# Performance work log

Measured on AMD Instinct MI355X. Metric: run time of the kernel, lower is better.

The kernel has to match this reference:

```python
import jax, jax.numpy as jnp
import numpy as np

B, P, D, H, L = 16384, 16, 49, 8, 6
NUM_CLASSES = 10
EPS = 1e-5


def _layernorm(x, w, b):
    mu = jnp.mean(x, axis=-1, keepdims=True)
    var = jnp.mean(jnp.square(x - mu), axis=-1, keepdims=True)
    return (x - mu) * jax.lax.rsqrt(var + EPS) * w + b


def setup_inputs() -> dict:
    key = jax.random.key(0)
    ks = iter(jax.random.split(key, 64))
    s = 0.05
    inp = {
        "x": jax.random.normal(next(ks), (B, P, D), jnp.float32),
        "trg": jax.random.randint(next(ks), (B,), 0, NUM_CLASSES, jnp.int32),
        "patch_proj_w": jax.random.normal(next(ks), (D, D)) * s,
        "patch_proj_b": jnp.zeros((D,)),
        "pos_enc": jax.random.normal(next(ks), (1, P, D)) * 0.02,
        # per-head per-layer attention weights, each head uses full dim D (as in source)
        "Wq": jax.random.normal(next(ks), (L, H, D, D)) * s,
        "bq": jnp.zeros((L, H, D)),
        "Wk": jax.random.normal(next(ks), (L, H, D, D)) * s,
        "bk": jnp.zeros((L, H, D)),
        "Wv": jax.random.normal(next(ks), (L, H, D, D)) * s,
        "bv": jnp.zeros((L, H, D)),
        "Wh": jax.random.normal(next(ks), (L, H, D, D)) * s,
        "bh": jnp.zeros((L, H, D)),
        "Wo": jax.random.normal(next(ks), (L, H * D, D)) * s,
        "bo": jnp.zeros((L, D)),
        "ln1_w": jnp.ones((L, D)), "ln1_b": jnp.zeros((L, D)),
        "ln2_w": jnp.ones((L, D)), "ln2_b": jnp.zeros((L, D)),
        "ffn1_w": jax.random.normal(next(ks), (L, D, 4 * D)) * s,
        "ffn1_b": jnp.zeros((L, 4 * D)),
        "ffn2_w": jax.random.normal(next(ks), (L, 4 * D, D)) * s,
        "ffn2_b": jnp.zeros((L, D)),
        "mlp_w1": jax.random.normal(next(ks), (D, D)) * s, "mlp_b1": jnp.zeros((D,)),
        "mlp_w2": jax.random.normal(next(ks), (D, D)) * s, "mlp_b2": jnp.zeros((D,)),
        "cls_w1": jax.random.normal(next(ks), (D, 25)) * s, "cls_b1": jnp.zeros((25,)),
        "cls_w2": jax.random.normal(next(ks), (25, NUM_CLASSES)) * s, "cls_b2": jnp.zeros((NUM_CLASSES,)),
    }
    return inp


def reference(x, trg, patch_proj_w, patch_proj_b, pos_enc,
              Wq, bq, Wk, bk, Wv, bv, Wh, bh, Wo, bo,
              ln1_w, ln1_b, ln2_w, ln2_b,
              ffn1_w, ffn1_b, ffn2_w, ffn2_b,
              mlp_w1, mlp_b1, mlp_w2, mlp_b2,
              cls_w1, cls_b1, cls_w2, cls_b2):
    b, p, d = x.shape
    h = x @ patch_proj_w + patch_proj_b + pos_enc[:, :p, :]
    scale = 1.0 / jnp.sqrt(jnp.float32(d))  # d_k = dim_proj = 49 per head
    for l in range(Wq.shape[0]):
        # all 8 heads batched: [b,p,d] x [h,d,e] -> [b,h,p,e]
        Q = jnp.einsum('bpd,hde->bhpe', h, Wq[l]) + bq[l][None, :, None, :]
        K = jnp.einsum('bpd,hde->bhpe', h, Wk[l]) + bk[l][None, :, None, :]
        V = jnp.einsum('bpd,hde->bhpe', h, Wv[l]) + bv[l][None, :, None, :]
        attn = jax.nn.softmax(jnp.einsum('bhpe,bhqe->bhpq', Q, K) * scale, axis=-1)
        ao = jnp.einsum('bhpq,bhqe->bhpe', attn, V)
        ho = jnp.einsum('bhpe,heo->bhpo', ao, Wh[l]) + bh[l][None, :, None, :]
        concat = ho.transpose(0, 2, 1, 3).reshape(b, p, -1)  # head-order concat
        attn_out = concat @ Wo[l] + bo[l]
        y = _layernorm(h + attn_out, ln1_w[l], ln1_b[l])
        ffn = jax.nn.gelu(y @ ffn1_w[l] + ffn1_b[l], approximate=False) @ ffn2_w[l] + ffn2_b[l]
        h = _layernorm(y + ffn, ln2_w[l], ln2_b[l])
        # mlp_between_blocks (shared weights) applied after every block
        h = (h @ mlp_w1 + mlp_b1) @ mlp_w2 + mlp_b2
    pooled = h.mean(axis=1)
    logits = (pooled @ cls_w1 + cls_b1) @ cls_w2 + cls_b2
    logp = jax.nn.log_softmax(logits, axis=-1)
    loss = -jnp.mean(jnp.take_along_axis(logp, trg[:, None].astype(jnp.int32), axis=-1))
    acc = jnp.mean((jnp.argmax(logits, axis=-1) == trg).astype(jnp.float32))
    return loss, acc
```

## Files before the change

### kernel.cpp

```cpp
#include <hip/hip_runtime.h>
#include <hip/hip_bf16.h>

#define DEV __device__ __forceinline__

typedef __attribute__((ext_vector_type(8))) __bf16 bfrag;
typedef __attribute__((ext_vector_type(4))) float  f32x4;

DEV f32x4 mfma32(bfrag a, bfrag b, f32x4 c) {
    return __builtin_amdgcn_mfma_f32_16x16x32_bf16(a, b, c, 0, 0, 0);
}

DEV unsigned short to_bf16(float f) {
    union { __bf16 b; unsigned short u; } cv;
    cv.b = (__bf16)f;
    return cv.u;
}

DEV float bf2f(unsigned short u) {
    union { unsigned int i; float f; } cv;
    cv.i = (unsigned int)u << 16;
    return cv.f;
}

#if defined(__has_builtin)
#if __has_builtin(__builtin_amdgcn_cvt_pk_bf16_f32)
#define HAS_PK_BF16 1
#endif
#endif

DEV unsigned int pk2(float a, float b) {
#ifdef HAS_PK_BF16
    auto r = __builtin_amdgcn_cvt_pk_bf16_f32(a, b);
    unsigned int u;
    __builtin_memcpy(&u, &r, 4);
    return u;
#else
    return (unsigned)to_bf16(a) | ((unsigned)to_bf16(b) << 16);
#endif
}

DEV void store4(unsigned short* p, float v0, float v1, float v2, float v3) {
    typedef __attribute__((ext_vector_type(2))) unsigned int uint2v;
    uint2v q;
    q[0] = pk2(v0, v1);
    q[1] = pk2(v2, v3);
    *reinterpret_cast<uint2v*>(p) = q;
}

DEV float fastrcp(float x) { float r; asm("v_rcp_f32 %0, %1" : "=v"(r) : "v"(x)); return r; }

DEV float gelu(float x) {
    float u = x * fmaf(0.07135481f, x * x, 1.5957691f);
    float e = __expf(-u);
    return x * fastrcp(1.0f + e);
}

namespace cfg {
constexpr size_t OFF_ACC  = 0;
constexpr size_t OFF_WQ   = 512;
constexpr size_t SZ_HEAD  = (size_t)48 * 64 * 64 * 2;
constexpr size_t OFF_WK   = OFF_WQ + SZ_HEAD;
constexpr size_t OFF_WV   = OFF_WK + SZ_HEAD;
constexpr size_t OFF_WHOO = OFF_WV + SZ_HEAD;
constexpr size_t OFF_F1   = OFF_WHOO + SZ_HEAD;
constexpr size_t OFF_F2   = OFF_F1 + (size_t)6 * 208 * 64 * 2;
constexpr size_t OFF_MF   = OFF_F2 + (size_t)6 * 64 * 224 * 2;
constexpr size_t OFF_PP   = OFF_MF + 8192;
constexpr size_t OFF_POSB = OFF_PP + 8192;
}


__global__ void pack_qk(const float* __restrict__ wq, const float* __restrict__ bq,
                        const float* __restrict__ wk, const float* __restrict__ bk,
                        char* __restrict__ ws)
{
    int id = blockIdx.x * 256 + threadIdx.x;
    int lh = id >> 12, pos = id & 4095;
    int n = pos >> 6, k = pos & 63;
    float s = 0.f;
// ... 89 lines not shown
            else if (k == 49) v = f1b[l * 196 + n];
        }
        ((unsigned short*)(ws + cfg::OFF_F1))[id] = to_bf16(v);
        return;
    }
    id -= 6 * 208 * 64;
    if (id < 6 * 64 * 224) {
        int l = id / (64 * 224), rem = id % (64 * 224), n = rem / 224, k = rem % 224;
        float v = 0.f;
        if (n < 49) {
            if (k < 196)       v = f2w[((size_t)l * 196 + k) * 49 + n];
            else if (k == 196) v = f2b[l * 49 + n];
        }
        ((unsigned short*)(ws + cfg::OFF_F2))[id] = to_bf16(v);
        return;
    }
    id -= 6 * 64 * 224;
    if (id < 4096) {
        int n = id >> 6, k = id & 63;
        ((unsigned short*)(ws + cfg::OFF_PP))[id] = to_bf16((n < 49 && k < 49) ? ppw[k * 49 + n] : 0.f);
        return;
    }
    id -= 4096;
    if (id < 1024) {
        int p = id >> 6, e = id & 63;
        ((float*)(ws + cfg::OFF_POSB))[id] = (e < 49) ? pos[p * 49 + e] + ppb[e] : 0.f;
        return;
    }
    id -= 1024;
    if (id < 128) ((float*)(ws + cfg::OFF_ACC))[id] = 0.f;
}


__global__ __launch_bounds__(64, 2)
void vit_main(const float* __restrict__ x, const int* __restrict__ trg,
              const float* __restrict__ cw1, const float* __restrict__ cb1,
              const float* __restrict__ cw2, const float* __restrict__ cb2,
              char* __restrict__ ws)
{
    constexpr int S64 = 72;
    constexpr int SV  = 40;
    constexpr int SP  = 40;
    constexpr int SM  = 232;
    constexpr int TA = 0, TB = 1152, TV = 2304, TP = 4384, MIDO = 1152, EL = 5024;
    __shared__ unsigned short sm[2 * EL];

    const int lane = threadIdx.x;
    const int g = lane >> 4, c = lane & 15;
    const long e0 = (long)blockIdx.x * 2;
    const f32x4 FZ = {0.f, 0.f, 0.f, 0.f};

    const unsigned short* WQK = (const unsigned short*)(ws + cfg::OFF_WQ);
    const unsigned short* WVO = (const unsigned short*)(ws + cfg::OFF_WK);
    const unsigned short* F1 = (const unsigned short*)(ws + cfg::OFF_F1);
    const unsigned short* F2 = (const unsigned short*)(ws + cfg::OFF_F2);
    const unsigned short* MF = (const unsigned short*)(ws + cfg::OFF_MF);
    const unsigned short* PP = (const unsigned short*)(ws + cfg::OFF_PP);
    const float* POSB = (const float*)(ws + cfg::OFF_POSB);
    float* ACC = (float*)(ws + cfg::OFF_ACC);

    #pragma unroll
    for (int u = 0; u < 2; ++u) {
        const float* xb = x + (e0 + u) * 784;
        #pragma unroll
        for (int it = 0; it < 8; ++it) {
            int i = it * 64 + lane;
            int p = i >> 5, ee = (i & 31) * 2;
            float v0 = (ee < 49) ? xb[p * 49 + ee] : 0.f;
            float v1 = (ee + 1 < 49) ? xb[p * 49 + ee + 1] : 0.f;
            *reinterpret_cast<unsigned int*>(&sm[u * EL + TA + p * S64 + ee]) = pk2(v0, v1);
        }
    }
    if (lane < 24) {
        int u2 = lane / 12, r = lane % 12, row = 12 + r / 3, seg = r % 3;
        *(f32x4*)&sm[u2 * EL + TP + row * SP + 16 + seg * 8] = FZ;
    }

    bfrag a_h[2][2];
    auto loadB = [&](int off, bfrag (&af)[2][2]) {
        #pragma unroll
        for (int u = 0; u < 2; ++u)
            #pragma unroll
            for (int kk = 0; kk < 2; ++kk)
                af[u][kk] = *(const bfrag*)&sm[u * EL + off + c * S64 + kk * 32 + g * 8];
    };
    loadB(TA, a_h);

    f32x4 hreg[2][4];
    #pragma unroll
    for (int mt = 0; mt < 4; ++mt) {
        f32x4 t0 = FZ, t1 = FZ;
        #pragma unroll
        for (int kk = 0; kk < 2; ++kk) {
            bfrag w = *(const bfrag*)&PP[(mt * 16 + c) * 64 + kk * 32 + g * 8];
            t0 = mfma32(w, a_h[0][kk], t0);
            t1 = mfma32(w, a_h[1][kk], t1);
        }
        f32x4 pb = *(const f32x4*)&POSB[c * 64 + mt * 16 + 4 * g];
        hreg[0][mt] = t0 + pb;
        hreg[1][mt] = t1 + pb;
    }

    for (int l = 0; l < 6; ++l) {
        #pragma unroll
        for (int u = 0; u < 2; ++u)
            #pragma unroll
            for (int mt = 0; mt < 4; ++mt)
                store4(&sm[u * EL + TA + c * S64 + mt * 16 + 4 * g],
                       hreg[u][mt][0], hreg[u][mt][1], hreg[u][mt][2], hreg[u][mt][3]);
        if (lane < 32) sm[(lane >> 4) * EL + TA + (lane & 15) * S64 + 49] = 0x3F80;
        loadB(TA, a_h);

        #pragma unroll
        for (int u = 0; u < 2; ++u) {
            *(f32x4*)&sm[u * EL + TV + lane * SV + 16] = FZ;
            *(f32x4*)&sm[u * EL + TV + lane * SV + 24] = FZ;
        }

        f32x4 oacc[2][4];
        #pragma unroll
        for (int u = 0; u < 2; ++u)
            #pragma unroll
            for (int mt = 0; mt < 4; ++mt) oacc[u][mt] = FZ;

        for (int hh = 0; hh < 8; ++hh) {
            const int lh = l * 8 + hh;
            const unsigned short* wqk = WQK + (size_t)lh * 4096;
            const unsigned short* wvo = WVO + (size_t)lh * 4096;

            #pragma unroll
            for (int mt = 0; mt < 4; ++mt) {
                f32x4 t0 = FZ, t1 = FZ;
                #pragma unroll
                for (int kk = 0; kk < 2; ++kk) {
                    bfrag wf = *(const bfrag*)&wqk[(mt * 16 + c) * 64 + kk * 32 + g * 8];
                    t0 = mfma32(wf, a_h[0][kk], t0);
                    t1 = mfma32(wf, a_h[1][kk], t1);
                }
                store4(&sm[0 * EL + TB + c * S64 + mt * 16 + 4 * g], t0[0], t0[1], t0[2], t0[3]);
                store4(&sm[1 * EL + TB + c * S64 + mt * 16 + 4 * g], t1[0], t1[1], t1[2], t1[3]);
            }
            #pragma unroll
            for (int nt = 0; nt < 4; ++nt) {
                f32x4 v0 = FZ, v1 = FZ;
                #pragma unroll
                for (int kk = 0; kk < 2; ++kk) {
                    bfrag wvf = *(const bfrag*)&wvo[(nt * 16 + c) * 64 + kk * 32 + g * 8];
                    v0 = mfma32(a_h[0][kk], wvf, v0);
                    v1 = mfma32(a_h[1][kk], wvf, v1);
                }
                store4(&sm[0 * EL + TV + (nt * 16 + c) * SV + 4 * g], v0[0], v0[1], v0[2], v0[3]);
                store4(&sm[1 * EL + TV + (nt * 16 + c) * SV + 4 * g], v1[0], v1[1], v1[2], v1[3]);
            }

            #pragma unroll
            for (int u = 0; u < 2; ++u) {
                f32x4 sc = FZ;
                #pragma unroll
                for (int kk = 0; kk < 2; ++kk) {
                    bfrag akf = *(const bfrag*)&sm[u * EL + TB + c * S64 + kk * 32 + g * 8];
                    sc = mfma32(akf, a_h[u][kk], sc);
                }
                float s0 = sc[0], s1 = sc[1], s2 = sc[2], s3 = sc[3];
                float m = fmaxf(fmaxf(s0, s1), fmaxf(s2, s3));
                m = fmaxf(m, __shfl_xor(m, 16));
                m = fmaxf(m, __shfl_xor(m, 32));
                float p0 = __expf(s0 - m), p1 = __expf(s1 - m);
                float p2 = __expf(s2 - m), p3 = __expf(s3 - m);
                float t = p0 + p1 + p2 + p3;
                t += __shfl_xor(t, 16);
                t += __shfl_xor(t, 32);
                float inv = fastrcp(t);
                store4(&sm[u * EL + TP + c * SP + 4 * g], p0 * inv, p1 * inv, p2 * inv, p3 * inv);
            }

            #pragma unroll
            for (int u = 0; u < 2; ++u) {
                bfrag bp = *(const bfrag*)&sm[u * EL + TP + c * SP + g * 8];
                #pragma unroll
                for (int mt = 0; mt < 4; ++mt) {
                    bfrag uf = *(const bfrag*)&sm[u * EL + TV + (mt * 16 + c) * SV + g * 8];
                    oacc[u][mt] = mfma32(uf, bp, oacc[u][mt]);
                }
            }
        }

        f32x4 yreg[2][4];
        {
            const float* ln1wp = (const float*)(ws + cfg::OFF_POSB + 4096);
            const float* ln1bp = ln1wp + 384;
            #pragma unroll
            for (int u = 0; u < 2; ++u) {
                float z[4][4];
                float s = 0.f, q2 = 0.f;
                #pragma unroll
                for (int mt = 0; mt < 4; ++mt)
                    #pragma unroll
                    for (int r = 0; r < 4; ++r) {
                        float zz = hreg[u][mt][r] + oacc[u][mt][r];
                        z[mt][r] = zz;
                        s += zz;
                        q2 += zz * zz;
                    }
                s += __shfl_xor(s, 16); s += __shfl_xor(s, 32);
                q2 += __shfl_xor(q2, 16); q2 += __shfl_xor(q2, 32);
                float mu = s * (1.f / 49.f);
                float var = q2 * (1.f / 49.f) - mu * mu;
                float rstd = rsqrtf(var + 1e-5f);
                #pragma unroll
                for (int mt = 0; mt < 4; ++mt) {
                    f32x4 lwv = *(const f32x4*)&ln1wp[l * 64 + mt * 16 + 4 * g];
                    f32x4 lbv = *(const f32x4*)&ln1bp[l * 64 + mt * 16 + 4 * g];
                    #pragma unroll
                    for (int r = 0; r < 4; ++r)
                        yreg[u][mt][r] = (z[mt][r] - mu) * rstd * lwv[r] + lbv[r];
                    store4(&sm[u * EL + TA + c * S64 + mt * 16 + 4 * g],
                           yreg[u][mt][0], yreg[u][mt][1], yreg[u][mt][2], yreg[u][mt][3]);
                }
            }
        }
        if (lane < 32) sm[(lane >> 4) * EL + TA + (lane & 15) * S64 + 49] = 0x3F80;

        {
            bfrag ay[2][2];
            loadB(TA, ay);
            {
                int u2 = lane >> 5, r5 = lane & 31, row = r5 >> 1, half = r5 & 1;
                *(f32x4*)&sm[u2 * EL + MIDO + row * SM + 208 + half * 8] = FZ;
            }
            const unsigned short* F1l = F1 + (size_t)l * 208 * 64;
            #pragma unroll
            for (int mt = 0; mt < 13; ++mt) {
                f32x4 m0 = FZ, m1 = FZ;
                #pragma unroll
                for (int kk = 0; kk < 2; ++kk) {
                    bfrag wf = *(const bfrag*)&F1l[(mt * 16 + c) * 64 + kk * 32 + g * 8];
                    m0 = mfma32(wf, ay[0][kk], m0);
                    m1 = mfma32(wf, ay[1][kk], m1);
                }
                store4(&sm[0 * EL + MIDO + c * SM + mt * 16 + 4 * g],
                       gelu(m0[0]), gelu(m0[1]), gelu(m0[2]), gelu(m0[3]));
                store4(&sm[1 * EL + MIDO + c * SM + mt * 16 + 4 * g],
                       gelu(m1[0]), gelu(m1[1]), gelu(m1[2]), gelu(m1[3]));
            }
            if (lane < 32) sm[(lane >> 4) * EL + MIDO + (lane & 15) * SM + 196] = 0x3F80;
        }

        {
            bfrag am[2][7];
            #pragma unroll
            for (int u = 0; u < 2; ++u)
                #pragma unroll
                for (int kk = 0; kk < 7; ++kk)
                    am[u][kk] = *(const bfrag*)&sm[u * EL + MIDO + c * SM + kk * 32 + g * 8];
            const unsigned short* F2l = F2 + (size_t)l * 64 * 224;
            f32x4 zac[2][4];
            #pragma unroll
            for (int mt = 0; mt < 4; ++mt) {
                f32x4 t0 = FZ, t1 = FZ;
                #pragma unroll
                for (int kk = 0; kk < 7; ++kk) {
                    bfrag wf = *(const bfrag*)&F2l[(mt * 16 + c) * 224 + kk * 32 + g * 8];
                    t0 = mfma32(wf, am[0][kk], t0);
                    t1 = mfma32(wf, am[1][kk], t1);
                }
                zac[0][mt] = t0; zac[1][mt] = t1;
            }
            const float* ln2wp = (const float*)(ws + cfg::OFF_POSB + 4096) + 768;
            const float* ln2bp = ln2wp + 384;
            #pragma unroll
            for (int u = 0; u < 2; ++u) {
                float z[4][4];
                float s = 0.f, q2 = 0.f;
                #pragma unroll
                for (int mt = 0; mt < 4; ++mt)
                    #pragma unroll
                    for (int r = 0; r < 4; ++r) {
                        float zz = yreg[u][mt][r] + zac[u][mt][r];
                        z[mt][r] = zz;
                        s += zz;
                        q2 += zz * zz;
                    }
                s += __shfl_xor(s, 16); s += __shfl_xor(s, 32);
                q2 += __shfl_xor(q2, 16); q2 += __shfl_xor(q2, 32);
                float mu = s * (1.f / 49.f);
                float var = q2 * (1.f / 49.f) - mu * mu;
                float rstd = rsqrtf(var + 1e-5f);
                #pragma unroll
                for (int mt = 0; mt < 4; ++mt) {
                    f32x4 lwv = *(const f32x4*)&ln2wp[l * 64 + mt * 16 + 4 * g];
                    f32x4 lbv = *(const f32x4*)&ln2bp[l * 64 + mt * 16 + 4 * g];
                    #pragma unroll
                    for (int r = 0; r < 4; ++r)
                        hreg[u][mt][r] = (z[mt][r] - mu) * rstd * lwv[r] + lbv[r];
                    store4(&sm[u * EL + TA + c * S64 + mt * 16 + 4 * g],
                           hreg[u][mt][0], hreg[u][mt][1], hreg[u][mt][2], hreg[u][mt][3]);
                }
            }
        }
        if (lane < 32) sm[(lane >> 4) * EL + TA + (lane & 15) * S64 + 49] = 0x3F80;

        {
            bfrag an[2][2];
            loadB(TA, an);
            #pragma unroll
            for (int mt = 0; mt < 4; ++mt) {
                f32x4 t0 = FZ, t1 = FZ;
                #pragma unroll
                for (int kk = 0; kk < 2; ++kk) {
                    bfrag wf = *(const bfrag*)&MF[(mt * 16 + c) * 64 + kk * 32 + g * 8];
                    t0 = mfma32(wf, an[0][kk], t0);
                    t1 = mfma32(wf, an[1][kk], t1);
                }
                hreg[0][mt] = t0;
                hreg[1][mt] = t1;
            }
        }
    }

    float loss_blk = 0.f, corr_blk = 0.f;
    #pragma unroll
    for (int u = 0; u < 2; ++u)
        #pragma unroll
        for (int mt = 0; mt < 4; ++mt)
            store4(&sm[u * EL + TA + c * S64 + mt * 16 + 4 * g],
                   hreg[u][mt][0], hreg[u][mt][1], hreg[u][mt][2], hreg[u][mt][3]);

    for (int u = 0; u < 2; ++u) {
        float s = 0.f;
        #pragma unroll
        for (int p = 0; p < 16; ++p)
            s += (float)(*reinterpret_cast<const __bf16*>(&sm[u * EL + TA + p * S64 + lane]));
        float* pf = reinterpret_cast<float*>(&sm[u * EL + TV]);
        pf[lane] = s * (1.f / 16.f);
        if (lane < 25) {
            float t = cb1[lane];
            for (int d2 = 0; d2 < 49; ++d2) t += pf[d2] * cw1[d2 * 25 + lane];
            pf[64 + lane] = t;
        }
        if (lane < 10) {
            float t2 = cb2[lane];
            for (int k2 = 0; k2 < 25; ++k2) t2 += pf[64 + k2] * cw2[k2 * 10 + lane];
            pf[96 + lane] = t2;
        }
        if (lane == 0) {
            float m = pf[96]; int am_ = 0;
            for (int j = 1; j < 10; ++j) if (pf[96 + j] > m) { m = pf[96 + j]; am_ = j; }
            float se = 0.f;
            for (int j = 0; j < 10; ++j) se += __expf(pf[96 + j] - m);
            float logZ = m + logf(se);
            int t = trg[e0 + u];
            loss_blk += logZ - pf[96 + t];
            corr_blk += (am_ == t) ? 1.f : 0.f;
        }
    }
    if (lane == 0) {
        int bin = blockIdx.x & 63;
        atomicAdd(&ACC[bin * 2 + 0], loss_blk);
        atomicAdd(&ACC[bin * 2 + 1], corr_blk);
    }
}

__global__ void pack_ln(const float* __restrict__ ln1w, const float* __restrict__ ln1b,
                        const float* __restrict__ ln2w, const float* __restrict__ ln2b,
                        char* __restrict__ ws)
{
    int id = blockIdx.x * 256 + threadIdx.x;
    if (id >= 1536) return;
    int which = id / 384, r = id % 384, l = r >> 6, f = r & 63;
    const float* s = (which == 0) ? ln1w : (which == 1) ? ln1b : (which == 2) ? ln2w : ln2b;
    float v = (f < 49) ? s[l * 49 + f] : 0.f;
    ((float*)(ws + cfg::OFF_POSB + 4096))[which * 384 + r] = v;
}

__global__ void finalize_k(const char* __restrict__ ws, float* __restrict__ out)
{
    const float* ACC = (const float*)(ws + cfg::OFF_ACC);
    int lane = threadIdx.x;
    float a = ACC[lane * 2 + 0];
    float b = ACC[lane * 2 + 1];
    for (int m = 1; m < 64; m <<= 1) {
        a += __shfl_xor(a, m);
        b += __shfl_xor(b, m);
    }
    if (lane == 0) {
        out[0] = a * (1.f / 16384.f);
        out[1] = b * (1.f / 16384.f);
    }
}


extern "C" void kernel_launch(void* const* d_in, const int* in_sizes, int n_in,
// ... 9 lines not shown
    const float* bq   = (const float*)d_in[6];
    const float* wk   = (const float*)d_in[7];
    const float* bk   = (const float*)d_in[8];
    const float* wv   = (const float*)d_in[9];
    const float* bv   = (const float*)d_in[10];
    const float* wh   = (const float*)d_in[11];
    const float* bh   = (const float*)d_in[12];
    const float* wo   = (const float*)d_in[13];
    const float* bo   = (const float*)d_in[14];
    const float* ln1w = (const float*)d_in[15];
    const float* ln1b = (const float*)d_in[16];
    const float* ln2w = (const float*)d_in[17];
    const float* ln2b = (const float*)d_in[18];
    const float* f1w  = (const float*)d_in[19];
    const float* f1b  = (const float*)d_in[20];
    const float* f2w  = (const float*)d_in[21];
    const float* f2b  = (const float*)d_in[22];
    const float* m1w  = (const float*)d_in[23];
    const float* m1b  = (const float*)d_in[24];
    const float* m2w  = (const float*)d_in[25];
    const float* m2b  = (const float*)d_in[26];
    const float* cw1  = (const float*)d_in[27];
    const float* cb1  = (const float*)d_in[28];
    const float* cw2  = (const float*)d_in[29];
    const float* cb2  = (const float*)d_in[30];
    char* ws = (char*)d_ws;

    pack_qk<<<768, 256, 0, stream>>>(wq, bq, wk, bk, ws);
    pack_v<<<768, 256, 0, stream>>>(wv, bv, ws);
    pack_fused<<<784, 256, 0, stream>>>(wh, bh, wo, bo, m1w, m1b, m2w, m2b, ws);
    pack_wvo<<<768, 256, 0, stream>>>(ws);
    pack_rest<<<669, 256, 0, stream>>>(f1w, f1b, f2w, f2b, ppw, ppb, pos, ws);
    pack_ln<<<6, 256, 0, stream>>>(ln1w, ln1b, ln2w, ln2b, ws);
    vit_main<<<16384 / 2, 64, 0, stream>>>(x, trg, cw1, cb1, cw2, cb2, ws);
    finalize_k<<<1, 64, 0, stream>>>(ws, (float*)d_out);
}
```

Measured before the change: 1.266 ms.

## Split per-block work across four wavefronts by output tile

The main kernel moves from one 64-lane wave per block to four waves, each owning one 16-column output tile of the projections, FFN and mixer matmuls. LayerNorm statistics are now combined across waves through a small shared reduction buffer, and softmax reuses the Q/K scratch region. The goal is more parallelism and less per-wave register pressure. The cost is many block-wide barriers per head and per layer, plus idle waves during the softmax and classifier stages.

```diff
diff --git a/kernel.cpp b/kernel.cpp
--- a/kernel.cpp
+++ b/kernel.cpp
@@ -200,7 +200,7 @@
 }
 
 
-__global__ __launch_bounds__(64, 2)
+__global__ __launch_bounds__(256, 4)
 void vit_main(const float* __restrict__ x, const int* __restrict__ trg,
               const float* __restrict__ cw1, const float* __restrict__ cb1,
               const float* __restrict__ cw2, const float* __restrict__ cb2,
@@ -208,12 +208,13 @@
 {
     constexpr int S64 = 72;
     constexpr int SV  = 40;
-    constexpr int SP  = 40;
     constexpr int SM  = 232;
-    constexpr int TA = 0, TB = 1152, TV = 2304, TP = 4384, MIDO = 1152, EL = 5024;
+    constexpr int TA = 0, TB = 1152, TV = 2304, MIDO = 1152, SCR = 4864, EL = 5376;
     __shared__ unsigned short sm[2 * EL];
 
-    const int lane = threadIdx.x;
+    const int tid  = threadIdx.x;
+    const int wid  = tid >> 6;
+    const int lane = tid & 63;
     const int g = lane >> 4, c = lane & 15;
     const long e0 = (long)blockIdx.x * 2;
     const f32x4 FZ = {0.f, 0.f, 0.f, 0.f};
@@ -226,23 +227,26 @@
     const unsigned short* PP = (const unsigned short*)(ws + cfg::OFF_PP);
     const float* POSB = (const float*)(ws + cfg::OFF_POSB);
     float* ACC = (float*)(ws + cfg::OFF_ACC);
-
-    #pragma unroll
-    for (int u = 0; u < 2; ++u) {
+    float* RED = (float*)(&sm[SCR]);
+
+    const float* ln1wp = (const float*)(ws + cfg::OFF_POSB + 4096);
+    const float* ln1bp = ln1wp + 384;
+    const float* ln2wp = ln1wp + 768;
+    const float* ln2bp = ln1wp + 1152;
+
+    {
+        int u = wid >> 1;
         const float* xb = x + (e0 + u) * 784;
         #pragma unroll
-        for (int it = 0; it < 8; ++it) {
-            int i = it * 64 + lane;
+        for (int t2 = 0; t2 < 4; ++t2) {
+            int i = ((wid & 1) * 4 + t2) * 64 + lane;
             int p = i >> 5, ee = (i & 31) * 2;
             float v0 = (ee < 49) ? xb[p * 49 + ee] : 0.f;
             float v1 = (ee + 1 < 49) ? xb[p * 49 + ee + 1] : 0.f;
             *reinterpret_cast<unsigned int*>(&sm[u * EL + TA + p * S64 + ee]) = pk2(v0, v1);
         }
     }
-    if (lane < 24) {
-        int u2 = lane / 12, r = lane % 12, row = 12 + r / 3, seg = r % 3;
-        *(f32x4*)&sm[u2 * EL + TP + row * SP + 16 + seg * 8] = FZ;
-    }
+    __syncthreads();
 
     bfrag a_h[2][2];
     auto loadB = [&](int off, bfrag (&af)[2][2]) {
@@ -254,75 +258,67 @@
     };
     loadB(TA, a_h);
 
-    f32x4 hreg[2][4];
-    #pragma unroll
-    for (int mt = 0; mt < 4; ++mt) {
+    f32x4 hreg[2];
+    {
         f32x4 t0 = FZ, t1 = FZ;
         #pragma unroll
         for (int kk = 0; kk < 2; ++kk) {
-            bfrag w = *(const bfrag*)&PP[(mt * 16 + c) * 64 + kk * 32 + g * 8];
+            bfrag w = *(const bfrag*)&PP[(wid * 16 + c) * 64 + kk * 32 + g * 8];
             t0 = mfma32(w, a_h[0][kk], t0);
             t1 = mfma32(w, a_h[1][kk], t1);
         }
-        f32x4 pb = *(const f32x4*)&POSB[c * 64 + mt * 16 + 4 * g];
-        hreg[0][mt] = t0 + pb;
-        hreg[1][mt] = t1 + pb;
+        f32x4 pb = *(const f32x4*)&POSB[c * 64 + wid * 16 + 4 * g];
+        hreg[0] = t0 + pb;
+        hreg[1] = t1 + pb;
     }
 
     for (int l = 0; l < 6; ++l) {
+        __syncthreads();
         #pragma unroll
         for (int u = 0; u < 2; ++u)
-            #pragma unroll
-            for (int mt = 0; mt < 4; ++mt)
-                store4(&sm[u * EL + TA + c * S64 + mt * 16 + 4 * g],
-                       hreg[u][mt][0], hreg[u][mt][1], hreg[u][mt][2], hreg[u][mt][3]);
-        if (lane < 32) sm[(lane >> 4) * EL + TA + (lane & 15) * S64 + 49] = 0x3F80;
+            store4(&sm[u * EL + TA + c * S64 + wid * 16 + 4 * g],
+                   hreg[u][0], hreg[u][1], hreg[u][2], hreg[u][3]);
+        if (wid == 3 && lane < 32) sm[(lane >> 4) * EL + TA + (lane & 15) * S64 + 49] = 0x3F80;
+        {
+            int u2 = wid >> 1, half = wid & 1;
+            *(f32x4*)&sm[u2 * EL + TV + lane * SV + 16 + half * 8] = FZ;
+        }
+        __syncthreads();
         loadB(TA, a_h);
 
-        #pragma unroll
-        for (int u = 0; u < 2; ++u) {
-            *(f32x4*)&sm[u * EL + TV + lane * SV + 16] = FZ;
-            *(f32x4*)&sm[u * EL + TV + lane * SV + 24] = FZ;
-        }
-
-        f32x4 oacc[2][4];
-        #pragma unroll
-        for (int u = 0; u < 2; ++u)
-            #pragma unroll
-            for (int mt = 0; mt < 4; ++mt) oacc[u][mt] = FZ;
+        f32x4 oacc[2];
+        oacc[0] = FZ; oacc[1] = FZ;
 
         for (int hh = 0; hh < 8; ++hh) {
             const int lh = l * 8 + hh;
             const unsigned short* wqk = WQK + (size_t)lh * 4096;
             const unsigned short* wvo = WVO + (size_t)lh * 4096;
 
-            #pragma unroll
-            for (int mt = 0; mt < 4; ++mt) {
+            {
                 f32x4 t0 = FZ, t1 = FZ;
                 #pragma unroll
                 for (int kk = 0; kk < 2; ++kk) {
-                    bfrag wf = *(const bfrag*)&wqk[(mt * 16 + c) * 64 + kk * 32 + g * 8];
+                    bfrag wf = *(const bfrag*)&wqk[(wid * 16 + c) * 64 + kk * 32 + g * 8];
                     t0 = mfma32(wf, a_h[0][kk], t0);
                     t1 = mfma32(wf, a_h[1][kk], t1);
                 }
-                store4(&sm[0 * EL + TB + c * S64 + mt * 16 + 4 * g], t0[0], t0[1], t0[2], t0[3]);
-                store4(&sm[1 * EL + TB + c * S64 + mt * 16 + 4 * g], t1[0], t1[1], t1[2], t1[3]);
-            }
-            #pragma unroll
-            for (int nt = 0; nt < 4; ++nt) {
+                store4(&sm[0 * EL + TB + c * S64 + wid * 16 + 4 * g], t0[0], t0[1], t0[2], t0[3]);
+                store4(&sm[1 * EL + TB + c * S64 + wid * 16 + 4 * g], t1[0], t1[1], t1[2], t1[3]);
+            }
+            {
                 f32x4 v0 = FZ, v1 = FZ;
                 #pragma unroll
                 for (int kk = 0; kk < 2; ++kk) {
-                    bfrag wvf = *(const bfrag*)&wvo[(nt * 16 + c) * 64 + kk * 32 + g * 8];
+                    bfrag wvf = *(const bfrag*)&wvo[(wid * 16 + c) * 64 + kk * 32 + g * 8];
                     v0 = mfma32(a_h[0][kk], wvf, v0);
                     v1 = mfma32(a_h[1][kk], wvf, v1);
                 }
-                store4(&sm[0 * EL + TV + (nt * 16 + c) * SV + 4 * g], v0[0], v0[1], v0[2], v0[3]);
-                store4(&sm[1 * EL + TV + (nt * 16 + c) * SV + 4 * g], v1[0], v1[1], v1[2], v1[3]);
-            }
-
-            #pragma unroll
-            for (int u = 0; u < 2; ++u) {
+                store4(&sm[0 * EL + TV + (wid * 16 + c) * SV + 4 * g], v0[0], v0[1], v0[2], v0[3]);
+                store4(&sm[1 * EL + TV + (wid * 16 + c) * SV + 4 * g], v1[0], v1[1], v1[2], v1[3]);
+            }
+            __syncthreads();
+            if (wid < 2) {
+                const int u = wid;
                 f32x4 sc = FZ;
                 #pragma unroll
                 for (int kk = 0; kk < 2; ++kk) {
@@ -339,162 +335,177 @@
                 t += __shfl_xor(t, 16);
                 t += __shfl_xor(t, 32);
                 float inv = fastrcp(t);
-                store4(&sm[u * EL + TP + c * SP + 4 * g], p0 * inv, p1 * inv, p2 * inv, p3 * inv);
-            }
-
+                store4(&sm[u * EL + TB + c * S64 + 4 * g], p0 * inv, p1 * inv, p2 * inv, p3 * inv);
+            }
+            __syncthreads();
             #pragma unroll
             for (int u = 0; u < 2; ++u) {
-                bfrag bp = *(const bfrag*)&sm[u * EL + TP + c * SP + g * 8];
-                #pragma unroll
-                for (int mt = 0; mt < 4; ++mt) {
-                    bfrag uf = *(const bfrag*)&sm[u * EL + TV + (mt * 16 + c) * SV + g * 8];
-                    oacc[u][mt] = mfma32(uf, bp, oacc[u][mt]);
-                }
-            }
-        }
-
-        f32x4 yreg[2][4];
+                bfrag bp = *(const bfrag*)&sm[u * EL + TB + c * S64 + g * 8];
+                bfrag uf = *(const bfrag*)&sm[u * EL + TV + (wid * 16 + c) * SV + g * 8];
+                oacc[u] = mfma32(uf, bp, oacc[u]);
+            }
+            __syncthreads();
+        }
+
+        f32x4 yreg[2];
         {
-            const float* ln1wp = (const float*)(ws + cfg::OFF_POSB + 4096);
-            const float* ln1bp = ln1wp + 384;
+            f32x4 zv[2];
+            float sA[2], qA[2];
             #pragma unroll
             for (int u = 0; u < 2; ++u) {
-                float z[4][4];
+                f32x4 z;
                 float s = 0.f, q2 = 0.f;
                 #pragma unroll
-                for (int mt = 0; mt < 4; ++mt)
-                    #pragma unroll
-                    for (int r = 0; r < 4; ++r) {
-                        float zz = hreg[u][mt][r] + oacc[u][mt][r];
-                        z[mt][r] = zz;
-                        s += zz;
-                        q2 += zz * zz;
-                    }
+                for (int r = 0; r < 4; ++r) {
+                    float t = hreg[u][r] + oacc[u][r];
+                    z[r] = t; s += t; q2 += t * t;
+                }
+                zv[u] = z;
                 s += __shfl_xor(s, 16); s += __shfl_xor(s, 32);
                 q2 += __shfl_xor(q2, 16); q2 += __shfl_xor(q2, 32);
-                float mu = s * (1.f / 49.f);
-                float var = q2 * (1.f / 49.f) - mu * mu;
+                sA[u] = s; qA[u] = q2;
+            }
+            if (lane < 16) {
+                #pragma unroll
+                for (int u = 0; u < 2; ++u) {
+                    RED[((wid * 2 + u) * 16 + lane) * 2 + 0] = sA[u];
+                    RED[((wid * 2 + u) * 16 + lane) * 2 + 1] = qA[u];
+                }
+            }
+            __syncthreads();
+            #pragma unroll
+            for (int u = 0; u < 2; ++u) {
+                float S = 0.f, Q = 0.f;
+                #pragma unroll
+                for (int w = 0; w < 4; ++w) {
+                    S += RED[((w * 2 + u) * 16 + c) * 2 + 0];
+                    Q += RED[((w * 2 + u) * 16 + c) * 2 + 1];
+                }
+                float mu = S * (1.f / 49.f);
+                float var = Q * (1.f / 49.f) - mu * mu;
                 float rstd = rsqrtf(var + 1e-5f);
-                #pragma unroll
-                for (int mt = 0; mt < 4; ++mt) {
-                    f32x4 lwv = *(const f32x4*)&ln1wp[l * 64 + mt * 16 + 4 * g];
-                    f32x4 lbv = *(const f32x4*)&ln1bp[l * 64 + mt * 16 + 4 * g];
-                    #pragma unroll
-                    for (int r = 0; r < 4; ++r)
-                        yreg[u][mt][r] = (z[mt][r] - mu) * rstd * lwv[r] + lbv[r];
-                    store4(&sm[u * EL + TA + c * S64 + mt * 16 + 4 * g],
-                           yreg[u][mt][0], yreg[u][mt][1], yreg[u][mt][2], yreg[u][mt][3]);
-                }
-            }
-        }
-        if (lane < 32) sm[(lane >> 4) * EL + TA + (lane & 15) * S64 + 49] = 0x3F80;
+                f32x4 lwv = *(const f32x4*)&ln1wp[l * 64 + wid * 16 + 4 * g];
+                f32x4 lbv = *(const f32x4*)&ln1bp[l * 64 + wid * 16 + 4 * g];
+                #pragma unroll
+                for (int r = 0; r < 4; ++r)
+                    yreg[u][r] = (zv[u][r] - mu) * rstd * lwv[r] + lbv[r];
+                store4(&sm[u * EL + TA + c * S64 + wid * 16 + 4 * g],
+                       yreg[u][0], yreg[u][1], yreg[u][2], yreg[u][3]);
+            }
+            if (wid == 3 && lane < 32) sm[(lane >> 4) * EL + TA + (lane & 15) * S64 + 49] = 0x3F80;
+        }
+        __syncthreads();
 
         {
             bfrag ay[2][2];
             loadB(TA, ay);
-            {
+            if (wid == 1) {
                 int u2 = lane >> 5, r5 = lane & 31, row = r5 >> 1, half = r5 & 1;
                 *(f32x4*)&sm[u2 * EL + MIDO + row * SM + 208 + half * 8] = FZ;
             }
             const unsigned short* F1l = F1 + (size_t)l * 208 * 64;
-            #pragma unroll
-            for (int mt = 0; mt < 13; ++mt) {
+            for (int m = wid; m < 13; m += 4) {
                 f32x4 m0 = FZ, m1 = FZ;
                 #pragma unroll
                 for (int kk = 0; kk < 2; ++kk) {
-                    bfrag wf = *(const bfrag*)&F1l[(mt * 16 + c) * 64 + kk * 32 + g * 8];
+                    bfrag wf = *(const bfrag*)&F1l[(m * 16 + c) * 64 + kk * 32 + g * 8];
                     m0 = mfma32(wf, ay[0][kk], m0);
                     m1 = mfma32(wf, ay[1][kk], m1);
                 }
-                store4(&sm[0 * EL + MIDO + c * SM + mt * 16 + 4 * g],
+                store4(&sm[0 * EL + MIDO + c * SM + m * 16 + 4 * g],
                        gelu(m0[0]), gelu(m0[1]), gelu(m0[2]), gelu(m0[3]));
-                store4(&sm[1 * EL + MIDO + c * SM + mt * 16 + 4 * g],
+                store4(&sm[1 * EL + MIDO + c * SM + m * 16 + 4 * g],
                        gelu(m1[0]), gelu(m1[1]), gelu(m1[2]), gelu(m1[3]));
             }
-            if (lane < 32) sm[(lane >> 4) * EL + MIDO + (lane & 15) * SM + 196] = 0x3F80;
-        }
+            if (wid == 0 && lane < 32) sm[(lane >> 4) * EL + MIDO + (lane & 15) * SM + 196] = 0x3F80;
+        }
+        __syncthreads();
 
         {
-            bfrag am[2][7];
-            #pragma unroll
-            for (int u = 0; u < 2; ++u)
-                #pragma unroll
-                for (int kk = 0; kk < 7; ++kk)
-                    am[u][kk] = *(const bfrag*)&sm[u * EL + MIDO + c * SM + kk * 32 + g * 8];
             const unsigned short* F2l = F2 + (size_t)l * 64 * 224;
-            f32x4 zac[2][4];
-            #pragma unroll
-            for (int mt = 0; mt < 4; ++mt) {
-                f32x4 t0 = FZ, t1 = FZ;
-                #pragma unroll
-                for (int kk = 0; kk < 7; ++kk) {
-                    bfrag wf = *(const bfrag*)&F2l[(mt * 16 + c) * 224 + kk * 32 + g * 8];
-                    t0 = mfma32(wf, am[0][kk], t0);
-                    t1 = mfma32(wf, am[1][kk], t1);
-                }
-                zac[0][mt] = t0; zac[1][mt] = t1;
-            }
-            const float* ln2wp = (const float*)(ws + cfg::OFF_POSB + 4096) + 768;
-            const float* ln2bp = ln2wp + 384;
+            f32x4 zac[2];
+            zac[0] = FZ; zac[1] = FZ;
+            #pragma unroll
+            for (int kk = 0; kk < 7; ++kk) {
+                bfrag wf = *(const bfrag*)&F2l[(wid * 16 + c) * 224 + kk * 32 + g * 8];
+                bfrag am0 = *(const bfrag*)&sm[0 * EL + MIDO + c * SM + kk * 32 + g * 8];
+                bfrag am1 = *(const bfrag*)&sm[1 * EL + MIDO + c * SM + kk * 32 + g * 8];
+                zac[0] = mfma32(wf, am0, zac[0]);
+                zac[1] = mfma32(wf, am1, zac[1]);
+            }
+            f32x4 zv[2];
+            float sA[2], qA[2];
             #pragma unroll
             for (int u = 0; u < 2; ++u) {
-                float z[4][4];
+                f32x4 z;
                 float s = 0.f, q2 = 0.f;
                 #pragma unroll
-                for (int mt = 0; mt < 4; ++mt)
-                    #pragma unroll
-                    for (int r = 0; r < 4; ++r) {
-                        float zz = yreg[u][mt][r] + zac[u][mt][r];
-                        z[mt][r] = zz;
-                        s += zz;
-                        q2 += zz * zz;
-                    }
+                for (int r = 0; r < 4; ++r) {
+                    float t = yreg[u][r] + zac[u][r];
+                    z[r] = t; s += t; q2 += t * t;
+                }
+                zv[u] = z;
                 s += __shfl_xor(s, 16); s += __shfl_xor(s, 32);
                 q2 += __shfl_xor(q2, 16); q2 += __shfl_xor(q2, 32);
-                float mu = s * (1.f / 49.f);
-                float var = q2 * (1.f / 49.f) - mu * mu;
+                sA[u] = s; qA[u] = q2;
+            }
+            if (lane < 16) {
+                #pragma unroll
+                for (int u = 0; u < 2; ++u) {
+                    RED[((wid * 2 + u) * 16 + lane) * 2 + 0] = sA[u];
+                    RED[((wid * 2 + u) * 16 + lane) * 2 + 1] = qA[u];
+                }
+            }
+            __syncthreads();
+            #pragma unroll
+            for (int u = 0; u < 2; ++u) {
+                float S = 0.f, Q = 0.f;
+                #pragma unroll
+                for (int w = 0; w < 4; ++w) {
+                    S += RED[((w * 2 + u) * 16 + c) * 2 + 0];
+                    Q += RED[((w * 2 + u) * 16 + c) * 2 + 1];
+                }
+                float mu = S * (1.f / 49.f);
+                float var = Q * (1.f / 49.f) - mu * mu;
                 float rstd = rsqrtf(var + 1e-5f);
-                #pragma unroll
-                for (int mt = 0; mt < 4; ++mt) {
-                    f32x4 lwv = *(const f32x4*)&ln2wp[l * 64 + mt * 16 + 4 * g];
-                    f32x4 lbv = *(const f32x4*)&ln2bp[l * 64 + mt * 16 + 4 * g];
-                    #pragma unroll
-                    for (int r = 0; r < 4; ++r)
-                        hreg[u][mt][r] = (z[mt][r] - mu) * rstd * lwv[r] + lbv[r];
-                    store4(&sm[u * EL + TA + c * S64 + mt * 16 + 4 * g],
-                           hreg[u][mt][0], hreg[u][mt][1], hreg[u][mt][2], hreg[u][mt][3]);
-                }
-            }
-        }
-        if (lane < 32) sm[(lane >> 4) * EL + TA + (lane & 15) * S64 + 49] = 0x3F80;
+                f32x4 lwv = *(const f32x4*)&ln2wp[l * 64 + wid * 16 + 4 * g];
+                f32x4 lbv = *(const f32x4*)&ln2bp[l * 64 + wid * 16 + 4 * g];
+                f32x4 hn;
+                #pragma unroll
+                for (int r = 0; r < 4; ++r)
+                    hn[r] = (zv[u][r] - mu) * rstd * lwv[r] + lbv[r];
+                hreg[u] = hn;
+                store4(&sm[u * EL + TA + c * S64 + wid * 16 + 4 * g],
+                       hn[0], hn[1], hn[2], hn[3]);
+            }
+            if (wid == 3 && lane < 32) sm[(lane >> 4) * EL + TA + (lane & 15) * S64 + 49] = 0x3F80;
+        }
+        __syncthreads();
 
         {
             bfrag an[2][2];
             loadB(TA, an);
-            #pragma unroll
-            for (int mt = 0; mt < 4; ++mt) {
-                f32x4 t0 = FZ, t1 = FZ;
-                #pragma unroll
-                for (int kk = 0; kk < 2; ++kk) {
-                    bfrag wf = *(const bfrag*)&MF[(mt * 16 + c) * 64 + kk * 32 + g * 8];
-                    t0 = mfma32(wf, an[0][kk], t0);
-                    t1 = mfma32(wf, an[1][kk], t1);
-                }
-                hreg[0][mt] = t0;
-                hreg[1][mt] = t1;
-            }
-        }
-    }
-
-    float loss_blk = 0.f, corr_blk = 0.f;
+            f32x4 t0 = FZ, t1 = FZ;
+            #pragma unroll
+            for (int kk = 0; kk < 2; ++kk) {
+                bfrag wf = *(const bfrag*)&MF[(wid * 16 + c) * 64 + kk * 32 + g * 8];
+                t0 = mfma32(wf, an[0][kk], t0);
+                t1 = mfma32(wf, an[1][kk], t1);
+            }
+            hreg[0] = t0;
+            hreg[1] = t1;
+        }
+    }
+
+    __syncthreads();
     #pragma unroll
     for (int u = 0; u < 2; ++u)
-        #pragma unroll
-        for (int mt = 0; mt < 4; ++mt)
-            store4(&sm[u * EL + TA + c * S64 + mt * 16 + 4 * g],
-                   hreg[u][mt][0], hreg[u][mt][1], hreg[u][mt][2], hreg[u][mt][3]);
-
-    for (int u = 0; u < 2; ++u) {
+        store4(&sm[u * EL + TA + c * S64 + wid * 16 + 4 * g],
+               hreg[u][0], hreg[u][1], hreg[u][2], hreg[u][3]);
+    __syncthreads();
+
+    if (wid < 2) {
+        const int u = wid;
         float s = 0.f;
         #pragma unroll
         for (int p = 0; p < 16; ++p)
@@ -518,14 +529,10 @@
             for (int j = 0; j < 10; ++j) se += __expf(pf[96 + j] - m);
             float logZ = m + logf(se);
             int t = trg[e0 + u];
-            loss_blk += logZ - pf[96 + t];
-            corr_blk += (am_ == t) ? 1.f : 0.f;
-        }
-    }
-    if (lane == 0) {
-        int bin = blockIdx.x & 63;
-        atomicAdd(&ACC[bin * 2 + 0], loss_blk);
-        atomicAdd(&ACC[bin * 2 + 1], corr_blk);
+            int bin = (int)((e0 + u) & 63);
+            atomicAdd(&ACC[bin * 2 + 0], logZ - pf[96 + t]);
+            atomicAdd(&ACC[bin * 2 + 1], (am_ == t) ? 1.f : 0.f);
+        }
     }
 }
 
@@ -601,6 +608,6 @@
     pack_wvo<<<768, 256, 0, stream>>>(ws);
     pack_rest<<<669, 256, 0, stream>>>(f1w, f1b, f2w, f2b, ppw, ppb, pos, ws);
     pack_ln<<<6, 256, 0, stream>>>(ln1w, ln1b, ln2w, ln2b, ws);
-    vit_main<<<16384 / 2, 64, 0, stream>>>(x, trg, cw1, cb1, cw2, cb2, ws);
+    vit_main<<<16384 / 2, 256, 0, stream>>>(x, trg, cw1, cb1, cw2, cb2, ws);
     finalize_k<<<1, 64, 0, stream>>>(ws, (float*)d_out);
 }
```

After: 1.339 ms. 5.8% more time.

## Double-buffer per-head attention weights in registers and reuse LDS for probabilities

Applied to the files above, without the earlier changes.

Each head's fused QK and VO weight fragments are now prefetched from global memory into registers one head ahead, and the head loop is fully unrolled, so weight loads overlap the current head's MFMA and softmax work. Launch bounds drop from two to one wave per SIMD to make room for the extra registers. The softmax probabilities now go into the Q·K scratch area instead of a separate padded buffer, which removes the zero-padding setup. The padding columns now hold stale scores, which the zeroed V padding cancels out. The cost is much higher register pressure and lower occupancy, so global latency is hidden by software prefetch instead of a second resident wave.

```diff
diff --git a/kernel.cpp b/kernel.cpp
--- a/kernel.cpp
+++ b/kernel.cpp
@@ -200,7 +200,7 @@
 }
 
 
-__global__ __launch_bounds__(64, 2)
+__global__ __launch_bounds__(64, 1)
 void vit_main(const float* __restrict__ x, const int* __restrict__ trg,
               const float* __restrict__ cw1, const float* __restrict__ cb1,
               const float* __restrict__ cw2, const float* __restrict__ cb2,
@@ -208,9 +208,8 @@
 {
     constexpr int S64 = 72;
     constexpr int SV  = 40;
-    constexpr int SP  = 40;
     constexpr int SM  = 232;
-    constexpr int TA = 0, TB = 1152, TV = 2304, TP = 4384, MIDO = 1152, EL = 5024;
+    constexpr int TA = 0, TB = 1152, TV = 2304, MIDO = 1152, EL = 5024;
     __shared__ unsigned short sm[2 * EL];
 
     const int lane = threadIdx.x;
@@ -227,6 +226,8 @@
     const float* POSB = (const float*)(ws + cfg::OFF_POSB);
     float* ACC = (float*)(ws + cfg::OFF_ACC);
 
+    const int wofs0 = c * 64 + g * 8;
+
     #pragma unroll
     for (int u = 0; u < 2; ++u) {
         const float* xb = x + (e0 + u) * 784;
@@ -239,10 +240,6 @@
             *reinterpret_cast<unsigned int*>(&sm[u * EL + TA + p * S64 + ee]) = pk2(v0, v1);
         }
     }
-    if (lane < 24) {
-        int u2 = lane / 12, r = lane % 12, row = 12 + r / 3, seg = r % 3;
-        *(f32x4*)&sm[u2 * EL + TP + row * SP + 16 + seg * 8] = FZ;
-    }
 
     bfrag a_h[2][2];
     auto loadB = [&](int off, bfrag (&af)[2][2]) {
@@ -270,6 +267,19 @@
     }
 
     for (int l = 0; l < 6; ++l) {
+        bfrag cwq[8], cwv[8];
+        {
+            const unsigned short* q0 = WQK + (size_t)(l * 8) * 4096;
+            const unsigned short* v0 = WVO + (size_t)(l * 8) * 4096;
+            #pragma unroll
+            for (int i = 0; i < 8; ++i) {
+                int o = (i >> 1) * 1024 + (i & 1) * 32 + wofs0;
+                cwq[i] = *(const bfrag*)&q0[o];
+                cwv[i] = *(const bfrag*)&v0[o];
+            }
+        }
+        __builtin_amdgcn_sched_barrier(0);
+
         #pragma unroll
         for (int u = 0; u < 2; ++u)
             #pragma unroll
@@ -291,19 +301,28 @@
             #pragma unroll
             for (int mt = 0; mt < 4; ++mt) oacc[u][mt] = FZ;
 
+        #pragma unroll
         for (int hh = 0; hh < 8; ++hh) {
-            const int lh = l * 8 + hh;
-            const unsigned short* wqk = WQK + (size_t)lh * 4096;
-            const unsigned short* wvo = WVO + (size_t)lh * 4096;
+            bfrag nwq[8], nwv[8];
+            if (hh < 7) {
+                const unsigned short* nq = WQK + (size_t)(l * 8 + hh + 1) * 4096;
+                const unsigned short* nv = WVO + (size_t)(l * 8 + hh + 1) * 4096;
+                #pragma unroll
+                for (int i = 0; i < 8; ++i) {
+                    int o = (i >> 1) * 1024 + (i & 1) * 32 + wofs0;
+                    nwq[i] = *(const bfrag*)&nq[o];
+                    nwv[i] = *(const bfrag*)&nv[o];
+                }
+                __builtin_amdgcn_sched_barrier(0);
+            }
 
             #pragma unroll
             for (int mt = 0; mt < 4; ++mt) {
                 f32x4 t0 = FZ, t1 = FZ;
                 #pragma unroll
                 for (int kk = 0; kk < 2; ++kk) {
-                    bfrag wf = *(const bfrag*)&wqk[(mt * 16 + c) * 64 + kk * 32 + g * 8];
-                    t0 = mfma32(wf, a_h[0][kk], t0);
-                    t1 = mfma32(wf, a_h[1][kk], t1);
+                    t0 = mfma32(cwq[mt * 2 + kk], a_h[0][kk], t0);
+                    t1 = mfma32(cwq[mt * 2 + kk], a_h[1][kk], t1);
                 }
                 store4(&sm[0 * EL + TB + c * S64 + mt * 16 + 4 * g], t0[0], t0[1], t0[2], t0[3]);
                 store4(&sm[1 * EL + TB + c * S64 + mt * 16 + 4 * g], t1[0], t1[1], t1[2], t1[3]);
@@ -313,9 +332,8 @@
                 f32x4 v0 = FZ, v1 = FZ;
                 #pragma unroll
                 for (int kk = 0; kk < 2; ++kk) {
-                    bfrag wvf = *(const bfrag*)&wvo[(nt * 16 + c) * 64 + kk * 32 + g * 8];
-                    v0 = mfma32(a_h[0][kk], wvf, v0);
-                    v1 = mfma32(a_h[1][kk], wvf, v1);
+                    v0 = mfma32(a_h[0][kk], cwv[nt * 2 + kk], v0);
+                    v1 = mfma32(a_h[1][kk], cwv[nt * 2 + kk], v1);
                 }
                 store4(&sm[0 * EL + TV + (nt * 16 + c) * SV + 4 * g], v0[0], v0[1], v0[2], v0[3]);
                 store4(&sm[1 * EL + TV + (nt * 16 + c) * SV + 4 * g], v1[0], v1[1], v1[2], v1[3]);
@@ -339,17 +357,22 @@
                 t += __shfl_xor(t, 16);
                 t += __shfl_xor(t, 32);
                 float inv = fastrcp(t);
-                store4(&sm[u * EL + TP + c * SP + 4 * g], p0 * inv, p1 * inv, p2 * inv, p3 * inv);
+                store4(&sm[u * EL + TB + c * S64 + 4 * g], p0 * inv, p1 * inv, p2 * inv, p3 * inv);
             }
 
             #pragma unroll
             for (int u = 0; u < 2; ++u) {
-                bfrag bp = *(const bfrag*)&sm[u * EL + TP + c * SP + g * 8];
+                bfrag bp = *(const bfrag*)&sm[u * EL + TB + c * S64 + g * 8];
                 #pragma unroll
                 for (int mt = 0; mt < 4; ++mt) {
                     bfrag uf = *(const bfrag*)&sm[u * EL + TV + (mt * 16 + c) * SV + g * 8];
                     oacc[u][mt] = mfma32(uf, bp, oacc[u][mt]);
                 }
+            }
+
+            if (hh < 7) {
+                #pragma unroll
+                for (int i = 0; i < 8; ++i) { cwq[i] = nwq[i]; cwv[i] = nwv[i]; }
             }
         }
 
```

Result: slower. 1.294 ms (+2.3%).

## Pass attention probabilities and V through lane shuffles and chunk the FFN

Applied to the files above, without the earlier changes.

The attention probabilities and the V tile are now repacked into MFMA operand fragments with cross-lane shuffles instead of being written to and read back from LDS. The FFN is restructured so that each pair of first-layer tiles is passed through GELU and immediately consumed by the second-layer MFMAs from a small LDS chunk, rather than materialising the full 224-wide intermediate. Together these shrink the per-block shared memory footprint from 5024 to 2304 elements per sample and cut LDS traffic, which may allow more resident waves. The cost is extra shuffle instructions and interleaved dependencies between the two FFN GEMMs.

```diff
diff --git a/kernel.cpp b/kernel.cpp
--- a/kernel.cpp
+++ b/kernel.cpp
@@ -5,6 +5,7 @@
 
 typedef __attribute__((ext_vector_type(8))) __bf16 bfrag;
 typedef __attribute__((ext_vector_type(4))) float  f32x4;
+typedef __attribute__((ext_vector_type(4))) unsigned int u32x4;
 
 DEV f32x4 mfma32(bfrag a, bfrag b, f32x4 c) {
     return __builtin_amdgcn_mfma_f32_16x16x32_bf16(a, b, c, 0, 0, 0);
@@ -45,6 +46,11 @@
     q[0] = pk2(v0, v1);
     q[1] = pk2(v2, v3);
     *reinterpret_cast<uint2v*>(p) = q;
+}
+
+DEV bfrag bf_from(unsigned int a, unsigned int b, unsigned int c, unsigned int d) {
+    u32x4 q; q[0] = a; q[1] = b; q[2] = c; q[3] = d;
+    bfrag r; __builtin_memcpy(&r, &q, 16); return r;
 }
 
 DEV float fastrcp(float x) { float r; asm("v_rcp_f32 %0, %1" : "=v"(r) : "v"(x)); return r; }
@@ -207,16 +213,18 @@
               char* __restrict__ ws)
 {
     constexpr int S64 = 72;
-    constexpr int SV  = 40;
-    constexpr int SP  = 40;
-    constexpr int SM  = 232;
-    constexpr int TA = 0, TB = 1152, TV = 2304, TP = 4384, MIDO = 1152, EL = 5024;
+    constexpr int VC  = 36;
+    constexpr int TA = 0, TB = 1152, EL = 2304;
     __shared__ unsigned short sm[2 * EL];
 
     const int lane = threadIdx.x;
     const int g = lane >> 4, c = lane & 15;
     const long e0 = (long)blockIdx.x * 2;
     const f32x4 FZ = {0.f, 0.f, 0.f, 0.f};
+
+    const int src0 = ((( 2 * g )     & 3) << 4) | c;
+    const int src1 = (((2 * g + 1) & 3) << 4) | c;
+    const bool glo = (g < 2);
 
     const unsigned short* WQK = (const unsigned short*)(ws + cfg::OFF_WQ);
     const unsigned short* WVO = (const unsigned short*)(ws + cfg::OFF_WK);
@@ -239,10 +247,6 @@
             *reinterpret_cast<unsigned int*>(&sm[u * EL + TA + p * S64 + ee]) = pk2(v0, v1);
         }
     }
-    if (lane < 24) {
-        int u2 = lane / 12, r = lane % 12, row = 12 + r / 3, seg = r % 3;
-        *(f32x4*)&sm[u2 * EL + TP + row * SP + 16 + seg * 8] = FZ;
-    }
 
     bfrag a_h[2][2];
     auto loadB = [&](int off, bfrag (&af)[2][2]) {
@@ -279,12 +283,6 @@
         if (lane < 32) sm[(lane >> 4) * EL + TA + (lane & 15) * S64 + 49] = 0x3F80;
         loadB(TA, a_h);
 
-        #pragma unroll
-        for (int u = 0; u < 2; ++u) {
-            *(f32x4*)&sm[u * EL + TV + lane * SV + 16] = FZ;
-            *(f32x4*)&sm[u * EL + TV + lane * SV + 24] = FZ;
-        }
-
         f32x4 oacc[2][4];
         #pragma unroll
         for (int u = 0; u < 2; ++u)
@@ -308,19 +306,8 @@
                 store4(&sm[0 * EL + TB + c * S64 + mt * 16 + 4 * g], t0[0], t0[1], t0[2], t0[3]);
                 store4(&sm[1 * EL + TB + c * S64 + mt * 16 + 4 * g], t1[0], t1[1], t1[2], t1[3]);
             }
-            #pragma unroll
-            for (int nt = 0; nt < 4; ++nt) {
-                f32x4 v0 = FZ, v1 = FZ;
-                #pragma unroll
-                for (int kk = 0; kk < 2; ++kk) {
-                    bfrag wvf = *(const bfrag*)&wvo[(nt * 16 + c) * 64 + kk * 32 + g * 8];
-                    v0 = mfma32(a_h[0][kk], wvf, v0);
-                    v1 = mfma32(a_h[1][kk], wvf, v1);
-                }
-                store4(&sm[0 * EL + TV + (nt * 16 + c) * SV + 4 * g], v0[0], v0[1], v0[2], v0[3]);
-                store4(&sm[1 * EL + TV + (nt * 16 + c) * SV + 4 * g], v1[0], v1[1], v1[2], v1[3]);
-            }
-
+
+            bfrag bp[2];
             #pragma unroll
             for (int u = 0; u < 2; ++u) {
                 f32x4 sc = FZ;
@@ -339,16 +326,34 @@
                 t += __shfl_xor(t, 16);
                 t += __shfl_xor(t, 32);
                 float inv = fastrcp(t);
-                store4(&sm[u * EL + TP + c * SP + 4 * g], p0 * inv, p1 * inv, p2 * inv, p3 * inv);
-            }
-
-            #pragma unroll
-            for (int u = 0; u < 2; ++u) {
-                bfrag bp = *(const bfrag*)&sm[u * EL + TP + c * SP + g * 8];
-                #pragma unroll
-                for (int mt = 0; mt < 4; ++mt) {
-                    bfrag uf = *(const bfrag*)&sm[u * EL + TV + (mt * 16 + c) * SV + g * 8];
-                    oacc[u][mt] = mfma32(uf, bp, oacc[u][mt]);
+                unsigned int pka = pk2(p0 * inv, p1 * inv);
+                unsigned int pkb = pk2(p2 * inv, p3 * inv);
+                unsigned int b0 = (unsigned)__shfl((int)pka, src0);
+                unsigned int b1 = (unsigned)__shfl((int)pkb, src0);
+                unsigned int b2 = (unsigned)__shfl((int)pka, src1);
+                unsigned int b3 = (unsigned)__shfl((int)pkb, src1);
+                bp[u] = bf_from(glo ? b0 : 0u, glo ? b1 : 0u,
+                                glo ? b2 : 0u, glo ? b3 : 0u);
+            }
+
+            #pragma unroll
+            for (int nt = 0; nt < 4; ++nt) {
+                bfrag wvf0 = *(const bfrag*)&wvo[(nt * 16 + c) * 64 + 0 * 32 + g * 8];
+                bfrag wvf1 = *(const bfrag*)&wvo[(nt * 16 + c) * 64 + 1 * 32 + g * 8];
+                #pragma unroll
+                for (int u = 0; u < 2; ++u) {
+                    f32x4 v = FZ;
+                    v = mfma32(a_h[u][0], wvf0, v);
+                    v = mfma32(a_h[u][1], wvf1, v);
+                    unsigned int va = pk2(v[0], v[1]);
+                    unsigned int vb = pk2(v[2], v[3]);
+                    unsigned int u0 = (unsigned)__shfl((int)va, src0);
+                    unsigned int u1 = (unsigned)__shfl((int)vb, src0);
+                    unsigned int u2 = (unsigned)__shfl((int)va, src1);
+                    unsigned int u3 = (unsigned)__shfl((int)vb, src1);
+                    bfrag uf = bf_from(glo ? u0 : 0u, glo ? u1 : 0u,
+                                       glo ? u2 : 0u, glo ? u3 : 0u);
+                    oacc[u][nt] = mfma32(uf, bp[u], oacc[u][nt]);
                 }
             }
         }
@@ -389,51 +394,54 @@
         }
         if (lane < 32) sm[(lane >> 4) * EL + TA + (lane & 15) * S64 + 49] = 0x3F80;
 
+        f32x4 zac[2][4];
+        #pragma unroll
+        for (int u = 0; u < 2; ++u)
+            #pragma unroll
+            for (int mt = 0; mt < 4; ++mt) zac[u][mt] = FZ;
         {
             bfrag ay[2][2];
             loadB(TA, ay);
-            {
-                int u2 = lane >> 5, r5 = lane & 31, row = r5 >> 1, half = r5 & 1;
-                *(f32x4*)&sm[u2 * EL + MIDO + row * SM + 208 + half * 8] = FZ;
-            }
             const unsigned short* F1l = F1 + (size_t)l * 208 * 64;
-            #pragma unroll
-            for (int mt = 0; mt < 13; ++mt) {
-                f32x4 m0 = FZ, m1 = FZ;
-                #pragma unroll
-                for (int kk = 0; kk < 2; ++kk) {
-                    bfrag wf = *(const bfrag*)&F1l[(mt * 16 + c) * 64 + kk * 32 + g * 8];
-                    m0 = mfma32(wf, ay[0][kk], m0);
-                    m1 = mfma32(wf, ay[1][kk], m1);
-                }
-                store4(&sm[0 * EL + MIDO + c * SM + mt * 16 + 4 * g],
-                       gelu(m0[0]), gelu(m0[1]), gelu(m0[2]), gelu(m0[3]));
-                store4(&sm[1 * EL + MIDO + c * SM + mt * 16 + 4 * g],
-                       gelu(m1[0]), gelu(m1[1]), gelu(m1[2]), gelu(m1[3]));
-            }
-            if (lane < 32) sm[(lane >> 4) * EL + MIDO + (lane & 15) * SM + 196] = 0x3F80;
+            const unsigned short* F2l = F2 + (size_t)l * 64 * 224;
+            #pragma unroll
+            for (int ci = 0; ci < 7; ++ci) {
+                #pragma unroll
+                for (int t = 0; t < 2; ++t) {
+                    const int mtile = ci * 2 + t;
+                    if (mtile < 13) {
+                        f32x4 m0 = FZ, m1 = FZ;
+                        #pragma unroll
+                        for (int kk = 0; kk < 2; ++kk) {
+                            bfrag wf = *(const bfrag*)&F1l[(mtile * 16 + c) * 64 + kk * 32 + g * 8];
+                            m0 = mfma32(wf, ay[0][kk], m0);
+                            m1 = mfma32(wf, ay[1][kk], m1);
+                        }
+                        store4(&sm[0 * EL + TB + c * VC + t * 16 + 4 * g],
+                               gelu(m0[0]), gelu(m0[1]), gelu(m0[2]), gelu(m0[3]));
+                        store4(&sm[1 * EL + TB + c * VC + t * 16 + 4 * g],
+                               gelu(m1[0]), gelu(m1[1]), gelu(m1[2]), gelu(m1[3]));
+                    } else {
+                        int u2 = lane >> 5, r5 = lane & 31, row = r5 >> 1, half = r5 & 1;
+                        *(f32x4*)&sm[u2 * EL + TB + row * VC + 16 + half * 8] = FZ;
+                    }
+                }
+                if (ci == 6) {
+                    if (lane < 32) sm[(lane >> 4) * EL + TB + (lane & 15) * VC + 4] = 0x3F80;
+                }
+                #pragma unroll
+                for (int u = 0; u < 2; ++u) {
+                    bfrag am = *(const bfrag*)&sm[u * EL + TB + c * VC + g * 8];
+                    #pragma unroll
+                    for (int mt = 0; mt < 4; ++mt) {
+                        bfrag wf = *(const bfrag*)&F2l[(mt * 16 + c) * 224 + ci * 32 + g * 8];
+                        zac[u][mt] = mfma32(wf, am, zac[u][mt]);
+                    }
+                }
+            }
         }
 
         {
-            bfrag am[2][7];
-            #pragma unroll
-            for (int u = 0; u < 2; ++u)
-                #pragma unroll
-                for (int kk = 0; kk < 7; ++kk)
-                    am[u][kk] = *(const bfrag*)&sm[u * EL + MIDO + c * SM + kk * 32 + g * 8];
-            const unsigned short* F2l = F2 + (size_t)l * 64 * 224;
-            f32x4 zac[2][4];
-            #pragma unroll
-            for (int mt = 0; mt < 4; ++mt) {
-                f32x4 t0 = FZ, t1 = FZ;
-                #pragma unroll
-                for (int kk = 0; kk < 7; ++kk) {
-                    bfrag wf = *(const bfrag*)&F2l[(mt * 16 + c) * 224 + kk * 32 + g * 8];
-                    t0 = mfma32(wf, am[0][kk], t0);
-                    t1 = mfma32(wf, am[1][kk], t1);
-                }
-                zac[0][mt] = t0; zac[1][mt] = t1;
-            }
             const float* ln2wp = (const float*)(ws + cfg::OFF_POSB + 4096) + 768;
             const float* ln2bp = ln2wp + 384;
             #pragma unroll
@@ -499,7 +507,7 @@
         #pragma unroll
         for (int p = 0; p < 16; ++p)
             s += (float)(*reinterpret_cast<const __bf16*>(&sm[u * EL + TA + p * S64 + lane]));
-        float* pf = reinterpret_cast<float*>(&sm[u * EL + TV]);
+        float* pf = reinterpret_cast<float*>(&sm[u * EL + TB]);
         pf[lane] = s * (1.f / 16.f);
         if (lane < 25) {
             float t = cb1[lane];
```

Measured after the change: 1.227 ms. -3.0%, faster.
